# Kernel tuning notes

Measured on AMD Instinct MI355X. Metric: run time of the kernel, lower is better.

## Reference

```python
import jax, jax.numpy as jnp
from jax import lax
import numpy as np

DIM = 256
D_STATE = 16
D_CONV = 4
EXPAND = 2
D_INNER = EXPAND * DIM          # 512
DT_RANK = (DIM + 15) // 16      # 16
EPS = 1e-5


def setup_inputs() -> dict:
    key = jax.random.key(0)
    ks = jax.random.split(key, 8)
    B, H, W = 8, 32, 32
    dt_init = 0.01  # softplus(b_dt) ~= dt_init at init (mamba-style)
    return {
        "x": jax.random.normal(ks[0], (B, DIM, H, W), jnp.float32),
        "ln_gamma": jnp.ones((DIM,), jnp.float32),
        "ln_beta": jnp.zeros((DIM,), jnp.float32),
        "W_in": jax.random.normal(ks[1], (DIM, 2 * D_INNER), jnp.float32) * 0.02,
        "conv_w": jax.random.normal(ks[2], (D_INNER, D_CONV), jnp.float32) * 0.2,
        "conv_b": jnp.zeros((D_INNER,), jnp.float32),
        "W_xproj": jax.random.normal(ks[3], (D_INNER, DT_RANK + 2 * D_STATE), jnp.float32) * 0.02,
        "W_dt": jax.random.normal(ks[4], (DT_RANK, D_INNER), jnp.float32) * 0.05,
        "b_dt": jnp.full((D_INNER,), float(np.log(np.expm1(dt_init))), jnp.float32),
        "A_log": jnp.log(jnp.broadcast_to(
            jnp.arange(1, D_STATE + 1, dtype=jnp.float32), (D_INNER, D_STATE))),
        "D_skip": jnp.ones((D_INNER,), jnp.float32),
        "W_out": jax.random.normal(ks[5], (D_INNER, DIM), jnp.float32) * 0.02,
    }


def _mamba_layer(x, ln_gamma, ln_beta, W_in, conv_w, conv_b, W_xproj,
                 W_dt, b_dt, A_log, D_skip, W_out):
    B, C, H, W = x.shape
    L = H * W
    # (B,C,H,W) -> (B, L, C)
    xf = x.transpose(0, 2, 3, 1).reshape(B, L, C)
    # LayerNorm over channel dim
    mu = xf.mean(-1, keepdims=True)
    var = ((xf - mu) ** 2).mean(-1, keepdims=True)
    xn = (xf - mu) * lax.rsqrt(var + EPS) * ln_gamma + ln_beta
    # in_proj -> u (ssm branch) and z (gate branch)
    xz = xn @ W_in                              # [B, L, 2*D_INNER]
    u, z = xz[..., :D_INNER], xz[..., D_INNER:]
    # causal depthwise conv1d over L, then SiLU
    uc = u.transpose(0, 2, 1)                   # [B, D_INNER, L]
    uc = lax.conv_general_dilated(
        uc, conv_w[:, None, :], window_strides=(1,),
        padding=[(D_CONV - 1, 0)], feature_group_count=D_INNER)
    u2 = jax.nn.silu(uc + conv_b[None, :, None]).transpose(0, 2, 1)  # [B, L, D_INNER]
    # input-dependent dt, B, C
    dbc = u2 @ W_xproj                          # [B, L, DT_RANK + 2*D_STATE]
    dt = jax.nn.softplus(dbc[..., :DT_RANK] @ W_dt + b_dt)            # [B, L, D_INNER]
    Bm = dbc[..., DT_RANK:DT_RANK + D_STATE]    # [B, L, D_STATE]
    Cm = dbc[..., DT_RANK + D_STATE:]           # [B, L, D_STATE]
    A = -jnp.exp(A_log)                         # [D_INNER, D_STATE]

    def step(h, ins):
        dt_t, B_t, C_t, u_t = ins               # [B,Din], [B,S], [B,S], [B,Din]
        dA = jnp.exp(dt_t[:, :, None] * A)      # [B, Din, S]
        h = dA * h + dt_t[:, :, None] * B_t[:, None, :] * u_t[:, :, None]
        y = jnp.einsum('bds,bs->bd', h, C_t)
        return h, y

    h0 = jnp.zeros((B, D_INNER, D_STATE), xf.dtype)
    xs = (dt.transpose(1, 0, 2), Bm.transpose(1, 0, 2),
          Cm.transpose(1, 0, 2), u2.transpose(1, 0, 2))
    _, ys = lax.scan(step, h0, xs)              # ys: [L, B, D_INNER]
    y = ys.transpose(1, 0, 2) + u2 * D_skip     # skip connection D*u
    y = y * jax.nn.silu(z)                      # gate
    o = y @ W_out                               # [B, L, C]
    return o.reshape(B, H, W, C).transpose(0, 3, 1, 2) + x


def reference(x, ln_gamma, ln_beta, W_in, conv_w, conv_b, W_xproj,
              W_dt, b_dt, A_log, D_skip, W_out):
    return _mamba_layer(x, ln_gamma, ln_beta, W_in, conv_w, conv_b, W_xproj,
                        W_dt, b_dt, A_log, D_skip, W_out)
```

## Files before the change

kernel.cpp:

```cpp
#include <hip/hip_runtime.h>
#include <hip/hip_bf16.h>
#include <math.h>

#define DIMC   256
#define DI     512
#define DS     16
#define DTR    16
#define NX     48
#define BATCH  8
#define LSEQ   1024
#define MROWS  8192
#define CHUNK  64
#define NC     (LSEQ / CHUNK)

typedef __attribute__((ext_vector_type(8))) short short8;
typedef __attribute__((ext_vector_type(4))) float f32x4;

__device__ __forceinline__ unsigned short f2bf(float v) {
  __hip_bfloat16 h = __float2bfloat16(v);
  return *reinterpret_cast<unsigned short*>(&h);
}
__device__ __forceinline__ float bf2f(unsigned short u) {
  return __int_as_float(((int)u) << 16);
}

__device__ __forceinline__ void load_lds16(const void* g, void* l) {
  __builtin_amdgcn_global_load_lds(
      (const __attribute__((address_space(1))) unsigned int*)g,
      (__attribute__((address_space(3))) unsigned int*)l, 16, 0, 0);
}

__device__ __forceinline__ float dpp_sum16(float v) {
  float t;
  t = __int_as_float(__builtin_amdgcn_mov_dpp(__float_as_int(v), 0xB1,  0xF, 0xF, true)); v += t;
  t = __int_as_float(__builtin_amdgcn_mov_dpp(__float_as_int(v), 0x4E,  0xF, 0xF, true)); v += t;
  t = __int_as_float(__builtin_amdgcn_mov_dpp(__float_as_int(v), 0x141, 0xF, 0xF, true)); v += t;
  t = __int_as_float(__builtin_amdgcn_mov_dpp(__float_as_int(v), 0x140, 0xF, 0xF, true)); v += t;
  return v;
}

__global__ __launch_bounds__(256) void prologue(const float* __restrict__ W_in,
                                                const float* __restrict__ W_out,
                                                const float* __restrict__ W_xproj,
                                                const float* __restrict__ W_dt,
                                                const float* __restrict__ x,
                                                const float* __restrict__ gamma,
                                                const float* __restrict__ beta,
                                                unsigned short* __restrict__ Wib,
                                                unsigned short* __restrict__ Wob,
                                                unsigned short* __restrict__ Wxpb,
                                                unsigned short* __restrict__ Wdtb,
                                                unsigned short* __restrict__ xnb) {
  __shared__ float sx[DIMC][67];
  __shared__ float smean[64], srs[64];
  const int blk = blockIdx.x, tid = threadIdx.x;
  if (blk < 384) {
    float (*t)[67] = sx;
    const float* W; unsigned short* Wt; int K, N, bx, by;
    if (blk < 256) { W = W_in;  Wt = Wib; K = DIMC; N = 1024; bx = blk & 31; by = blk >> 5; }
    else           { W = W_out; Wt = Wob; K = DI;   N = DIMC; bx = (blk - 256) & 7; by = (blk - 256) >> 3; }
    int n0 = bx * 32, k0 = by * 32;
    int tx = tid & 31, ty = tid >> 5;
    for (int i = ty; i < 32; i += 8) t[i][tx] = W[(size_t)(k0 + i) * N + n0 + tx];
    __syncthreads();
    for (int i = ty; i < 32; i += 8)
      Wt[(size_t)(n0 + i) * K + k0 + tx] = f2bf(t[tx][i]);
    return;
  }
  if (blk < 512) {
    int idx = (blk - 384) * 256 + tid;
    int n = idx >> 9, k = idx & 511;
    Wxpb[idx] = (n < NX) ? f2bf(W_xproj[(size_t)k * NX + n]) : (unsigned short)0;
    return;
  }
  if (blk < 576) {
    int idx = (blk - 512) * 256 + tid;
    int n = idx >> 5, k = idx & 31;
    Wdtb[idx] = (k < DTR) ? f2bf(W_dt[(size_t)k * DI + n]) : (unsigned short)0;
    return;
  }
  const int lb = blk - 576;
  const int b = lb >> 4, l0 = (lb & 15) * 64;
  {
    const int cbase = tid >> 2;
    const int lp = (tid & 3) * 16;
#pragma unroll
    for (int cg = 0; cg < 4; ++cg) {
      const int c = cg * 64 + cbase;
      const float* p = x + ((size_t)b * DIMC + c) * LSEQ + l0 + lp;
#pragma unroll
      for (int q = 0; q < 4; ++q) {
        float4 v = *(const float4*)(p + q * 4);
        sx[c][lp + q * 4 + 0] = v.x;
        sx[c][lp + q * 4 + 1] = v.y;
        sx[c][lp + q * 4 + 2] = v.z;
        sx[c][lp + q * 4 + 3] = v.w;
      }
    }
  }
  __syncthreads();
  {
    const int lane = tid & 63, w = tid >> 6;
    const int l = (w << 4) + (lane & 15);
    const int quad = lane >> 4;
    float sum = 0.f, sq = 0.f;
#pragma unroll 8
    for (int cc = 0; cc < 64; ++cc) {
      float v = sx[quad * 64 + cc][l];
      sum += v; sq += v * v;
    }
    sum += __shfl_xor(sum, 16); sq += __shfl_xor(sq, 16);
    sum += __shfl_xor(sum, 32); sq += __shfl_xor(sq, 32);
    if (quad == 0) {
      float mean = sum * (1.f / 256.f);
      float var  = sq * (1.f / 256.f) - mean * mean;
      smean[l] = mean; srs[l] = rsqrtf(var + 1e-5f);
    }
  }
  __syncthreads();
  {
    const float gg = gamma[tid], bb = beta[tid];
    const size_t base = ((size_t)b * LSEQ + l0) * DIMC + tid;
#pragma unroll 4
    for (int ll = 0; ll < 64; ++ll) {
      float v = (sx[tid][ll] - smean[ll]) * srs[ll] * gg + bb;
      xnb[base + (size_t)ll * DIMC] = f2bf(v);
    }
  }
}

#define GTM 128
#define GTN 64
#define GBK 32
__global__ __launch_bounds__(256) void gemm_bf16(const unsigned short* __restrict__ A,
                                                 const unsigned short* __restrict__ Bt,
                                                 void* __restrict__ Cout,
                                                 int M, int N, int K, int mode,
                                                 const float* __restrict__ X) {
  __shared__ unsigned short As[GTM][GBK];
  __shared__ unsigned short Bs[GTN][GBK];
  const int tid = threadIdx.x;
  const int lane = tid & 63, wave = tid >> 6;
  const int wm = wave >> 1, wn = wave & 1;
  const int quad = lane >> 4, l16 = lane & 15;
  const int m0 = blockIdx.y * GTM, n0 = blockIdx.x * GTN;

  f32x4 acc[4][2];
#pragma unroll
  for (int i = 0; i < 4; ++i)
#pragma unroll
    for (int j = 0; j < 2; ++j) acc[i][j] = (f32x4){0.f, 0.f, 0.f, 0.f};

  for (int k0 = 0; k0 < K; k0 += GBK) {
#pragma unroll
    for (int q = 0; q < 2; ++q) {
      int id = q * 256 + tid;
      int row = id >> 2, c = id & 3;
      load_lds16(A + (size_t)(m0 + row) * K + k0 + c * 8,
                 (char*)&As[0][0] + (size_t)(q * 256 + wave * 64) * 16);
    }
    {
      int row = tid >> 2, c = tid & 3;
      load_lds16(Bt + (size_t)(n0 + row) * K + k0 + c * 8,
                 (char*)&Bs[0][0] + (size_t)(wave * 64) * 16);
    }
    __syncthreads();
    short8 af[4], bfrag[2];
#pragma unroll
    for (int i = 0; i < 4; ++i)
      af[i] = *(const short8*)&As[wm * 64 + i * 16 + l16][quad * 8];
#pragma unroll
    for (int j = 0; j < 2; ++j)
      bfrag[j] = *(const short8*)&Bs[wn * 32 + j * 16 + l16][quad * 8];
#pragma unroll
    for (int i = 0; i < 4; ++i)
#pragma unroll
      for (int j = 0; j < 2; ++j)
        acc[i][j] = __builtin_amdgcn_mfma_f32_16x16x32_bf16(af[i], bfrag[j], acc[i][j], 0, 0, 0);
    __syncthreads();
  }

  if (mode == 2) {
    unsigned short* Cb = (unsigned short*)Cout;
#pragma unroll
    for (int i = 0; i < 4; ++i) {
      int rowb = wm * 64 + i * 16 + quad * 4;
#pragma unroll
      for (int j = 0; j < 2; ++j) {
        int n = n0 + wn * 32 + j * 16 + l16;
#pragma unroll
        for (int r = 0; r < 4; ++r)
          Cb[(size_t)(m0 + rowb + r) * N + n] = f2bf(acc[i][j][r]);
      }
    }
  } else {
    float* C = (float*)Cout;
#pragma unroll
    for (int i = 0; i < 4; ++i) {
      int m = m0 + wm * 64 + i * 16 + quad * 4;
      int b = m >> 10, l = m & 1023;
#pragma unroll
      for (int j = 0; j < 2; ++j) {
        int n = n0 + wn * 32 + j * 16 + l16;
        size_t o = (size_t)b * (DIMC * LSEQ) + (size_t)n * LSEQ + l;
        f32x4 xv = *(const f32x4*)(X + o);
        f32x4 rv = acc[i][j] + xv;
        *(f32x4*)(C + o) = rv;
      }
    }
  }
}

__global__ __launch_bounds__(256) void conv_xproj_dt(
    const unsigned short* __restrict__ xzb,
    const float* __restrict__ conv_w,
    const float* __restrict__ conv_b,
    const unsigned short* __restrict__ Wxpb,
    const unsigned short* __restrict__ Wdtb,
    const float* __restrict__ b_dt,
    float* __restrict__ dbcBC,
    unsigned int* __restrict__ dtu) {
  __shared__ unsigned short Bs[64][512 + 8];
  __shared__ unsigned short sxz[35][512];
  __shared__ unsigned short su[32][512 + 8];
  __shared__ unsigned short sdbc[32][40];
  const int m0 = blockIdx.x * 32;
  const int l0 = m0 & 1023;
  const int tid = threadIdx.x, lane = tid & 63, w = tid >> 6;
  const int quad = lane >> 4, l16 = lane & 15;

#pragma unroll
  for (int q = 0; q < 16; ++q) {
    int id = q * 256 + tid;
    int row = id >> 6, c8 = id & 63;
    *(uint4*)&Bs[row][c8 * 8] = *(const uint4*)(Wxpb + (size_t)row * 512 + c8 * 8);
  }
#pragma unroll
  for (int q = 0; q < 9; ++q) {
    int id = q * 256 + tid;
    if (id < 35 * 64) {
      int rr = id >> 6, c8 = id & 63;
      uint4 v; v.x = 0u; v.y = 0u; v.z = 0u; v.w = 0u;
      if (l0 - 3 + rr >= 0)
        v = *(const uint4*)(xzb + (size_t)(m0 - 3 + rr) * 1024 + c8 * 8);
      *(uint4*)&sxz[rr][c8 * 8] = v;
    }
  }
  __syncthreads();

#pragma unroll 4
  for (int q = 0; q < 64; ++q) {
    int idx = q * 256 + tid;
    int r = idx >> 9, c = idx & 511;
    float4 wv = *(const float4*)(conv_w + c * 4);
    float acc = conv_b[c];
    acc = fmaf(bf2f(sxz[r + 0][c]), wv.x, acc);
    acc = fmaf(bf2f(sxz[r + 1][c]), wv.y, acc);
    acc = fmaf(bf2f(sxz[r + 2][c]), wv.z, acc);
    acc = fmaf(bf2f(sxz[r + 3][c]), wv.w, acc);
    float u = acc / (1.f + __expf(-acc));
    su[r][c] = f2bf(u);
  }
  __syncthreads();

  f32x4 acc[2];
  acc[0] = (f32x4){0.f, 0.f, 0.f, 0.f};
  acc[1] = (f32x4){0.f, 0.f, 0.f, 0.f};
#pragma unroll 4
  for (int k0 = 0; k0 < 512; k0 += 32) {
    short8 af0 = *(const short8*)&su[l16][k0 + quad * 8];
    short8 af1 = *(const short8*)&su[16 + l16][k0 + quad * 8];
    short8 bf  = *(const short8*)&Bs[w * 16 + l16][k0 + quad * 8];
    acc[0] = __builtin_amdgcn_mfma_f32_16x16x32_bf16(af0, bf, acc[0], 0, 0, 0);
    acc[1] = __builtin_amdgcn_mfma_f32_16x16x32_bf16(af1, bf, acc[1], 0, 0, 0);
  }
  if (w == 1 || w == 2) {
#pragma unroll
    for (int i = 0; i < 2; ++i)
#pragma unroll
      for (int r = 0; r < 4; ++r)
        dbcBC[(size_t)(m0 + i * 16 + quad * 4 + r) * 32 + (w - 1) * 16 + l16] = acc[i][r];
  }
  if (w < 2) {
#pragma unroll
    for (int i = 0; i < 2; ++i)
#pragma unroll
      for (int r = 0; r < 4; ++r)
        sdbc[i * 16 + quad * 4 + r][w * 16 + l16] = f2bf(acc[i][r]);
  }
  __syncthreads();

  short8 af0 = *(const short8*)&sdbc[l16][quad * 8];
  short8 af1 = *(const short8*)&sdbc[16 + l16][quad * 8];
#pragma unroll
  for (int jn = 0; jn < 8; ++jn) {
    const int n0 = w * 128 + jn * 16;
    short8 bf = *(const short8*)(Wdtb + (size_t)(n0 + l16) * 32 + quad * 8);
    f32x4 a0 = (f32x4){0.f, 0.f, 0.f, 0.f}, a1 = a0;
    a0 = __builtin_amdgcn_mfma_f32_16x16x32_bf16(af0, bf, a0, 0, 0, 0);
    a1 = __builtin_amdgcn_mfma_f32_16x16x32_bf16(af1, bf, a1, 0, 0, 0);
    const float bd = b_dt[n0 + l16];
#pragma unroll
    for (int r = 0; r < 4; ++r) {
      int lr0 = quad * 4 + r;
      int lr1 = lr0 + 16;
      float v = a0[r] + bd;
      float sp = (v > 20.f) ? v : log1pf(__expf(v));
      unsigned int u0 = (unsigned int)su[lr0][n0 + l16];
      dtu[(size_t)(m0 + lr0) * DI + n0 + l16] = u0 | ((unsigned int)f2bf(sp) << 16);
      float v2 = a1[r] + bd;
      float sp2 = (v2 > 20.f) ? v2 : log1pf(__expf(v2));
      unsigned int u1 = (unsigned int)su[lr1][n0 + l16];
      dtu[(size_t)(m0 + lr1) * DI + n0 + l16] = u1 | ((unsigned int)f2bf(sp2) << 16);
    }
  }
}

__global__ __launch_bounds__(256) void scan_pass1(const unsigned int* __restrict__ dtu,
                                                  const float* __restrict__ dbcBC,
                                                  const float* __restrict__ A_log,
                                                  float* __restrict__ hend,
                                                  float* __restrict__ Ssum) {
  const int bb = blockIdx.x, dblk = blockIdx.y, cc = blockIdx.z;
  const int tid = threadIdx.x;
  const int di = tid >> 4, s = tid & 15;
  const int d = dblk * 16 + di;
  const float Ads = -__expf(A_log[d * DS + s]);

  __shared__ float2 sdu[CHUNK][18];
  __shared__ float  sB[CHUNK][17];
  {
    const int t0 = cc * CHUNK;
    int lin = tid * 4;
    int tt = lin >> 4, dd = lin & 15;
    size_t m = (size_t)bb * LSEQ + t0 + tt;
    uint4 du4 = *(const uint4*)(dtu + m * DI + dblk * 16 + dd);
    f32x4 a, b2;
    a[0]  = bf2f((unsigned short)(du4.x >> 16)); a[1]  = bf2f((unsigned short)(du4.x & 0xffff));
    a[2]  = bf2f((unsigned short)(du4.y >> 16)); a[3]  = bf2f((unsigned short)(du4.y & 0xffff));
    b2[0] = bf2f((unsigned short)(du4.z >> 16)); b2[1] = bf2f((unsigned short)(du4.z & 0xffff));
    b2[2] = bf2f((unsigned short)(du4.w >> 16)); b2[3] = bf2f((unsigned short)(du4.w & 0xffff));
    *(f32x4*)&sdu[tt][dd]     = a;
    *(f32x4*)&sdu[tt][dd + 2] = b2;
    f32x4 Bv = *(const f32x4*)(dbcBC + m * 32 + dd);
    *(f32x4*)&sB[tt][dd] = Bv;
  }
  __syncthreads();
  float h = 0.f, dtsum = 0.f;
#pragma unroll 4
  for (int tt = 0; tt < CHUNK; ++tt) {
    float2 du = sdu[tt][di];
    float Bv  = sB[tt][s];
    h = fmaf(__expf(du.x * Ads), h, du.x * du.y * Bv);
    dtsum += du.x;
  }
  size_t ci = ((size_t)(bb * NC + cc) * DI + d);
  hend[ci * DS + s] = h;
  if (s == 0) Ssum[ci] = dtsum;
}

__global__ __launch_bounds__(256) void scan_pass2(const float* __restrict__ A_log,
                                                  const float* __restrict__ hend,
                                                  const float* __restrict__ Ssum,
                                                  float* __restrict__ hin) {
  const int bb = blockIdx.x, dblk = blockIdx.y;
  const int tid = threadIdx.x;
  const int di = tid >> 4, s = tid & 15;
  const int d = dblk * 16 + di;
  const float Ads = -__expf(A_log[d * DS + s]);
  float h = 0.f;
  for (int cc = 0; cc < NC; ++cc) {
    size_t ci = ((size_t)(bb * NC + cc) * DI + d);
    hin[ci * DS + s] = h;
    h = fmaf(__expf(Ads * Ssum[ci]), h, hend[ci * DS + s]);
  }
}

__global__ __launch_bounds__(256) void scan_pass3(const unsigned int* __restrict__ dtu,
                                                  const float* __restrict__ dbcBC,
                                                  const unsigned short* __restrict__ xzb,
                                                  const float* __restrict__ A_log,
                                                  const float* __restrict__ D_skip,
                                                  const float* __restrict__ hin,
                                                  unsigned short* __restrict__ yb) {
  const int bb = blockIdx.x, dblk = blockIdx.y, cc = blockIdx.z;
  const int tid = threadIdx.x;
  const int di = tid >> 4, s = tid & 15;
  const int d = dblk * 16 + di;
  const float Ads = -__expf(A_log[d * DS + s]);

  __shared__ float2 sdu[CHUNK][18];
  __shared__ float2 sBC[CHUNK][18];
  __shared__ float  sy[CHUNK][16];
  const int t0 = cc * CHUNK;
  const size_t mbase = (size_t)bb * LSEQ + t0;
  {
    int lin = tid * 4;
    int tt = lin >> 4, dd = lin & 15;
    size_t m = mbase + tt;
    uint4 du4 = *(const uint4*)(dtu + m * DI + dblk * 16 + dd);
    f32x4 a, b2;
    a[0]  = bf2f((unsigned short)(du4.x >> 16)); a[1]  = bf2f((unsigned short)(du4.x & 0xffff));
    a[2]  = bf2f((unsigned short)(du4.y >> 16)); a[3]  = bf2f((unsigned short)(du4.y & 0xffff));
    b2[0] = bf2f((unsigned short)(du4.z >> 16)); b2[1] = bf2f((unsigned short)(du4.z & 0xffff));
    b2[2] = bf2f((unsigned short)(du4.w >> 16)); b2[3] = bf2f((unsigned short)(du4.w & 0xffff));
    *(f32x4*)&sdu[tt][dd]     = a;
    *(f32x4*)&sdu[tt][dd + 2] = b2;
    f32x4 Bv = *(const f32x4*)(dbcBC + m * 32 + dd);
    f32x4 Cv = *(const f32x4*)(dbcBC + m * 32 + 16 + dd);
    f32x4 p0, p1;
    p0[0] = Bv[0]; p0[1] = Cv[0]; p0[2] = Bv[1]; p0[3] = Cv[1];
    p1[0] = Bv[2]; p1[1] = Cv[2]; p1[2] = Bv[3]; p1[3] = Cv[3];
    *(f32x4*)&sBC[tt][dd]     = p0;
    *(f32x4*)&sBC[tt][dd + 2] = p1;
  }
  __syncthreads();
  float h = hin[((size_t)(bb * NC + cc) * DI + d) * DS + s];
#pragma unroll 4
  for (int tt = 0; tt < CHUNK; ++tt) {
    float2 du = sdu[tt][di];
    float2 bc = sBC[tt][s];
    h = fmaf(__expf(du.x * Ads), h, du.x * du.y * bc.x);
    float v = dpp_sum16(h * bc.y);
    if (s == 0) sy[tt][di] = v;
  }
  __syncthreads();
#pragma unroll
  for (int q = 0; q < 4; ++q) {
    int lin = q * 256 + tid;
    int tt = lin >> 4, dd = lin & 15;
    size_t m = mbase + tt;
    float z = bf2f(xzb[m * 1024 + DI + dblk * 16 + dd]);
    float yv = sy[tt][dd] + sdu[tt][dd].y * D_skip[dblk * 16 + dd];
    yv *= z / (1.f + __expf(-z));
    yb[m * DI + dblk * 16 + dd] = f2bf(yv);
  }
}

extern "C" void kernel_launch(void* const* d_in, const int* in_sizes, int n_in,
                              void* d_out, int out_size, void* d_ws, size_t ws_size,
                              hipStream_t stream) {
  const float* x       = (const float*)d_in[0];
  const float* ln_g    = (const float*)d_in[1];
  const float* ln_b    = (const float*)d_in[2];
  const float* W_in    = (const float*)d_in[3];
  const float* conv_w  = (const float*)d_in[4];
  const float* conv_b  = (const float*)d_in[5];
  const float* W_xproj = (const float*)d_in[6];
  const float* W_dt    = (const float*)d_in[7];
  const float* b_dt    = (const float*)d_in[8];
  const float* A_log   = (const float*)d_in[9];
  const float* D_skip  = (const float*)d_in[10];
  const float* W_out   = (const float*)d_in[11];
  float* out = (float*)d_out;

  float* ws    = (float*)d_ws;
  float* dbcBC = ws;
  float* hend  = dbcBC + (size_t)MROWS * 32;
  float* hin   = hend + (size_t)BATCH * NC * DI * DS;
  float* Ssum  = hin  + (size_t)BATCH * NC * DI * DS;
  unsigned int* dtu = (unsigned int*)(Ssum + (size_t)BATCH * NC * DI);
  unsigned short* xzb  = (unsigned short*)(dtu + (size_t)MROWS * DI);
  unsigned short* yb   = xzb + (size_t)MROWS * 1024;
  unsigned short* xnb  = yb;
  unsigned short* Wib  = yb  + (size_t)MROWS * DI;
  unsigned short* Wob  = Wib + (size_t)DIMC * 1024;
  unsigned short* Wxpb = Wob + (size_t)DI * DIMC;
  unsigned short* Wdtb = Wxpb + (size_t)64 * 512;

  prologue<<<704, 256, 0, stream>>>(W_in, W_out, W_xproj, W_dt, x, ln_g, ln_b,
                                    Wib, Wob, Wxpb, Wdtb, xnb);

  gemm_bf16<<<dim3(1024 / GTN, MROWS / GTM), 256, 0, stream>>>(
      xnb, Wib, xzb, MROWS, 1024, DIMC, 2, nullptr);

  conv_xproj_dt<<<MROWS / 32, 256, 0, stream>>>(xzb, conv_w, conv_b,
                                                Wxpb, Wdtb, b_dt, dbcBC, dtu);

  dim3 gp13(BATCH, DI / 16, NC);
  dim3 gp2(BATCH, DI / 16);
  scan_pass1<<<gp13, 256, 0, stream>>>(dtu, dbcBC, A_log, hend, Ssum);
  scan_pass2<<<gp2, 256, 0, stream>>>(A_log, hend, Ssum, hin);
  scan_pass3<<<gp13, 256, 0, stream>>>(dtu, dbcBC, xzb, A_log, D_skip, hin, yb);

  gemm_bf16<<<dim3(DIMC / GTN, MROWS / GTM), 256, 0, stream>>>(
      yb, Wob, out, MROWS, DIMC, DI, 1, x);
}
```

Before: 191.5 us.

## Use 128x128 GEMM tile for in_proj and shrink conv_xproj_dt row tile

Adds a dedicated 128x128-tile bf16 MFMA GEMM for the input projection, giving each wave a 4x4 accumulator block for more operand reuse per LDS load. conv_xproj_dt now handles 16 rows per block instead of 32. It reads the x_proj weights straight from global memory instead of staging all of them in LDS, which cuts LDS use and should raise occupancy and block count. The trade-off is more redundant global weight reads, since each block now re-reads the weight rows it needs, and higher register pressure in the larger GEMM tile.

```diff
diff --git a/kernel.cpp b/kernel.cpp
--- a/kernel.cpp
+++ b/kernel.cpp
@@ -129,6 +129,68 @@
   }
 }
 
+__global__ __launch_bounds__(256) void gemm_bf16_128(const unsigned short* __restrict__ A,
+                                                     const unsigned short* __restrict__ Bt,
+                                                     unsigned short* __restrict__ Cb,
+                                                     int M, int N, int K) {
+  __shared__ unsigned short As[128][32];
+  __shared__ unsigned short Bs[128][32];
+  const int tid = threadIdx.x;
+  const int lane = tid & 63, wave = tid >> 6;
+  const int wm = wave >> 1, wn = wave & 1;
+  const int quad = lane >> 4, l16 = lane & 15;
+  const int m0 = blockIdx.y * 128, n0 = blockIdx.x * 128;
+
+  f32x4 acc[4][4];
+#pragma unroll
+  for (int i = 0; i < 4; ++i)
+#pragma unroll
+    for (int j = 0; j < 4; ++j) acc[i][j] = (f32x4){0.f, 0.f, 0.f, 0.f};
+
+  for (int k0 = 0; k0 < K; k0 += 32) {
+#pragma unroll
+    for (int q = 0; q < 2; ++q) {
+      int id = q * 256 + tid;
+      int row = id >> 2, c = id & 3;
+      load_lds16(A + (size_t)(m0 + row) * K + k0 + c * 8,
+                 (char*)&As[0][0] + (size_t)(q * 256 + wave * 64) * 16);
+    }
+#pragma unroll
+    for (int q = 0; q < 2; ++q) {
+      int id = q * 256 + tid;
+      int row = id >> 2, c = id & 3;
+      load_lds16(Bt + (size_t)(n0 + row) * K + k0 + c * 8,
+                 (char*)&Bs[0][0] + (size_t)(q * 256 + wave * 64) * 16);
+    }
+    __syncthreads();
+    short8 af[4], bfr[4];
+#pragma unroll
+    for (int i = 0; i < 4; ++i)
+      af[i] = *(const short8*)&As[wm * 64 + i * 16 + l16][quad * 8];
+#pragma unroll
+    for (int j = 0; j < 4; ++j)
+      bfr[j] = *(const short8*)&Bs[wn * 64 + j * 16 + l16][quad * 8];
+#pragma unroll
+    for (int i = 0; i < 4; ++i)
+#pragma unroll
+      for (int j = 0; j < 4; ++j)
+        acc[i][j] = __builtin_amdgcn_mfma_f32_16x16x32_bf16(af[i], bfr[j], acc[i][j], 0, 0, 0);
+    __syncthreads();
+  }
+
+#pragma unroll
+  for (int i = 0; i < 4; ++i) {
+    int rowb = wm * 64 + i * 16 + quad * 4;
+#pragma unroll
+    for (int j = 0; j < 4; ++j) {
+      int n = n0 + wn * 64 + j * 16 + l16;
+#pragma unroll
+      for (int r = 0; r < 4; ++r)
+        Cb[(size_t)(m0 + rowb + r) * N + n] = f2bf(acc[i][j][r]);
+    }
+  }
+}
+
 #define GTM 128
 #define GTN 64
 #define GBK 32
@@ -220,25 +282,18 @@
     const float* __restrict__ b_dt,
     float* __restrict__ dbcBC,
     unsigned int* __restrict__ dtu) {
-  __shared__ unsigned short Bs[64][512 + 8];
-  __shared__ unsigned short sxz[35][512];
-  __shared__ unsigned short su[32][512 + 8];
-  __shared__ unsigned short sdbc[32][40];
-  const int m0 = blockIdx.x * 32;
+  __shared__ unsigned short sxz[19][512];
+  __shared__ unsigned short su[16][512 + 8];
+  __shared__ unsigned short sdbc[16][40];
+  const int m0 = blockIdx.x * 16;
   const int l0 = m0 & 1023;
   const int tid = threadIdx.x, lane = tid & 63, w = tid >> 6;
   const int quad = lane >> 4, l16 = lane & 15;
 
 #pragma unroll
-  for (int q = 0; q < 16; ++q) {
+  for (int q = 0; q < 5; ++q) {
     int id = q * 256 + tid;
-    int row = id >> 6, c8 = id & 63;
-    *(uint4*)&Bs[row][c8 * 8] = *(const uint4*)(Wxpb + (size_t)row * 512 + c8 * 8);
-  }
-#pragma unroll
-  for (int q = 0; q < 9; ++q) {
-    int id = q * 256 + tid;
-    if (id < 35 * 64) {
+    if (id < 19 * 64) {
       int rr = id >> 6, c8 = id & 63;
       uint4 v; v.x = 0u; v.y = 0u; v.z = 0u; v.w = 0u;
       if (l0 - 3 + rr >= 0)
@@ -249,7 +304,7 @@
   __syncthreads();
 
 #pragma unroll 4
-  for (int q = 0; q < 64; ++q) {
+  for (int q = 0; q < 32; ++q) {
     int idx = q * 256 + tid;
     int r = idx >> 9, c = idx & 511;
     float4 wv = *(const float4*)(conv_w + c * 4);
@@ -263,55 +318,40 @@
   }
   __syncthreads();
 
-  f32x4 acc[2];
-  acc[0] = (f32x4){0.f, 0.f, 0.f, 0.f};
-  acc[1] = (f32x4){0.f, 0.f, 0.f, 0.f};
+  f32x4 acc = (f32x4){0.f, 0.f, 0.f, 0.f};
 #pragma unroll 4
   for (int k0 = 0; k0 < 512; k0 += 32) {
-    short8 af0 = *(const short8*)&su[l16][k0 + quad * 8];
-    short8 af1 = *(const short8*)&su[16 + l16][k0 + quad * 8];
-    short8 bf  = *(const short8*)&Bs[w * 16 + l16][k0 + quad * 8];
-    acc[0] = __builtin_amdgcn_mfma_f32_16x16x32_bf16(af0, bf, acc[0], 0, 0, 0);
-    acc[1] = __builtin_amdgcn_mfma_f32_16x16x32_bf16(af1, bf, acc[1], 0, 0, 0);
+    short8 af = *(const short8*)&su[l16][k0 + quad * 8];
+    short8 bf = *(const short8*)(Wxpb + (size_t)(w * 16 + l16) * 512 + k0 + quad * 8);
+    acc = __builtin_amdgcn_mfma_f32_16x16x32_bf16(af, bf, acc, 0, 0, 0);
   }
   if (w == 1 || w == 2) {
 #pragma unroll
-    for (int i = 0; i < 2; ++i)
-#pragma unroll
-      for (int r = 0; r < 4; ++r)
-        dbcBC[(size_t)(m0 + i * 16 + quad * 4 + r) * 32 + (w - 1) * 16 + l16] = acc[i][r];
+    for (int r = 0; r < 4; ++r)
+      dbcBC[(size_t)(m0 + quad * 4 + r) * 32 + (w - 1) * 16 + l16] = acc[r];
   }
   if (w < 2) {
 #pragma unroll
-    for (int i = 0; i < 2; ++i)
-#pragma unroll
-      for (int r = 0; r < 4; ++r)
-        sdbc[i * 16 + quad * 4 + r][w * 16 + l16] = f2bf(acc[i][r]);
+    for (int r = 0; r < 4; ++r)
+      sdbc[quad * 4 + r][w * 16 + l16] = f2bf(acc[r]);
   }
   __syncthreads();
 
   short8 af0 = *(const short8*)&sdbc[l16][quad * 8];
-  short8 af1 = *(const short8*)&sdbc[16 + l16][quad * 8];
 #pragma unroll
   for (int jn = 0; jn < 8; ++jn) {
     const int n0 = w * 128 + jn * 16;
     short8 bf = *(const short8*)(Wdtb + (size_t)(n0 + l16) * 32 + quad * 8);
-    f32x4 a0 = (f32x4){0.f, 0.f, 0.f, 0.f}, a1 = a0;
+    f32x4 a0 = (f32x4){0.f, 0.f, 0.f, 0.f};
     a0 = __builtin_amdgcn_mfma_f32_16x16x32_bf16(af0, bf, a0, 0, 0, 0);
-    a1 = __builtin_amdgcn_mfma_f32_16x16x32_bf16(af1, bf, a1, 0, 0, 0);
     const float bd = b_dt[n0 + l16];
 #pragma unroll
     for (int r = 0; r < 4; ++r) {
       int lr0 = quad * 4 + r;
-      int lr1 = lr0 + 16;
       float v = a0[r] + bd;
       float sp = (v > 20.f) ? v : log1pf(__expf(v));
       unsigned int u0 = (unsigned int)su[lr0][n0 + l16];
       dtu[(size_t)(m0 + lr0) * DI + n0 + l16] = u0 | ((unsigned int)f2bf(sp) << 16);
-      float v2 = a1[r] + bd;
-      float sp2 = (v2 > 20.f) ? v2 : log1pf(__expf(v2));
-      unsigned int u1 = (unsigned int)su[lr1][n0 + l16];
-      dtu[(size_t)(m0 + lr1) * DI + n0 + l16] = u1 | ((unsigned int)f2bf(sp2) << 16);
     }
   }
 }
@@ -471,10 +511,10 @@
   prologue<<<704, 256, 0, stream>>>(W_in, W_out, W_xproj, W_dt, x, ln_g, ln_b,
                                     Wib, Wob, Wxpb, Wdtb, xnb);
 
-  gemm_bf16<<<dim3(1024 / GTN, MROWS / GTM), 256, 0, stream>>>(
-      xnb, Wib, xzb, MROWS, 1024, DIMC, 2, nullptr);
-
-  conv_xproj_dt<<<MROWS / 32, 256, 0, stream>>>(xzb, conv_w, conv_b,
+  gemm_bf16_128<<<dim3(1024 / 128, MROWS / 128), 256, 0, stream>>>(
+      xnb, Wib, xzb, MROWS, 1024, DIMC);
+
+  conv_xproj_dt<<<MROWS / 16, 256, 0, stream>>>(xzb, conv_w, conv_b,
                                                 Wxpb, Wdtb, b_dt, dbcBC, dtu);
 
   dim3 gp13(BATCH, DI / 16, NC);
```

New measurement: 185.4 us. 1.03x faster.
